# Optimization experiments

Measured on AMD Instinct MI355X. Metric: run time of the kernel, lower is better.

## Reference

```python
import jax, jax.numpy as jnp
import numpy as np

N, E, F, H, C, ED = 10000, 160000, 4, 32, 4, 2  # nodes, edges, in_feat, hidden, classes, edge_dim


def _init(key, shape, fan_in):
    return jax.random.normal(key, shape, jnp.float32) / np.float32(np.sqrt(fan_in))


def setup_inputs() -> dict:
    key = jax.random.key(0)
    ks = iter(jax.random.split(key, 40))
    inp = {
        "x": jax.random.normal(next(ks), (N, F), jnp.float32),
        "edge_index": jax.random.randint(next(ks), (2, E), 0, N, dtype=jnp.int32),
        "edge_attr": jax.random.normal(next(ks), (E, ED), jnp.float32),
    }
    for i, din in enumerate([F, H, H]):
        inp[f"w1_{i}"] = _init(next(ks), (ED, H), ED)
        inp[f"b1_{i}"] = jnp.zeros((H,), jnp.float32)
        inp[f"w2_{i}"] = _init(next(ks), (H, din * H), H)
        inp[f"b2_{i}"] = jnp.zeros((din * H,), jnp.float32)
        inp[f"root_{i}"] = _init(next(ks), (din, H), din)
        inp[f"bias_{i}"] = jnp.zeros((H,), jnp.float32)
    inp["fc_w"] = _init(next(ks), (H, C), H)
    inp["fc_b"] = jnp.zeros((C,), jnp.float32)
    return inp


def _nnconv(x, src, dst, edge_attr, w1, b1, w2, b2, root, bias):
    # edge MLP -> per-edge weight matrix [E, din, H]
    h = jax.nn.relu(edge_attr @ w1 + b1)                      # [E, H]
    W = (h @ w2 + b2).reshape(E, x.shape[1], -1)              # [E, din, H]
    msg = jnp.einsum('ei,eio->eo', x[src], W)                 # gather + per-edge matvec
    agg = jax.ops.segment_sum(msg, dst, num_segments=N)       # scatter-add to targets
    return agg + x @ root + bias                              # root weight + bias (NNConv)


def reference(x, edge_index, edge_attr,
              w1_0, b1_0, w2_0, b2_0, root_0, bias_0,
              w1_1, b1_1, w2_1, b2_1, root_1, bias_1,
              w1_2, b1_2, w2_2, b2_2, root_2, bias_2,
              fc_w, fc_b):
    src, dst = edge_index[0], edge_index[1]
    layers = [(w1_0, b1_0, w2_0, b2_0, root_0, bias_0),
              (w1_1, b1_1, w2_1, b2_1, root_1, bias_1),
              (w1_2, b1_2, w2_2, b2_2, root_2, bias_2)]
    for p in layers:
        x = jax.nn.relu(_nnconv(x, src, dst, edge_attr, *p))  # dropout=0 -> no-op
    logits = x @ fc_w + fc_b
    return jax.nn.log_softmax(logits, axis=1)
```

## Files before the change

kernel.cpp:

```cpp
#include <hip/hip_runtime.h>
#include <hip/hip_bf16.h>
#include <math.h>

#define N_NODES 10000
#define N_EDGES 160000

typedef __attribute__((ext_vector_type(8))) short bf16x8;
typedef __attribute__((ext_vector_type(4))) float f32x4;

static __device__ inline unsigned short f2b(float v) {
    __hip_bfloat16 b = __float2bfloat16(v);
    return *reinterpret_cast<unsigned short*>(&b);
}

__global__ __launch_bounds__(256) void k_tw2z(const float* __restrict__ s0,
                                              const float* __restrict__ s1,
                                              const float* __restrict__ s2,
                                              float* __restrict__ t0,
                                              float* __restrict__ t1,
                                              float* __restrict__ t2,
                                              int* __restrict__ cnt2) {
    int tid = blockIdx.x * 256 + threadIdx.x;
    if (tid < 20480) { cnt2[tid] = 0; return; }
    int d = tid - 20480;
    if (d < 4096) {
        int i = d >> 10, j = d & 1023, o = j >> 5, k = j & 31;
        t0[d] = s0[k * 128 + i * 32 + o];
    } else if (d < 4096 + 32768) {
        int q = d - 4096;
        int i = q >> 10, j = q & 1023, o = j >> 5, k = j & 31;
        t1[q] = s1[k * 1024 + i * 32 + o];
    } else if (d < 4096 + 65536) {
        int q = d - 4096 - 32768;
        int i = q >> 10, j = q & 1023, o = j >> 5, k = j & 31;
        t2[q] = s2[k * 1024 + i * 32 + o];
    }
}

__global__ __launch_bounds__(256) void k_hist(const int* __restrict__ ei,
                                              int* __restrict__ cnt_src,
                                              int* __restrict__ cnt_dst) {
    int e = blockIdx.x * 256 + threadIdx.x;
    if (e >= N_EDGES) return;
    atomicAdd(&cnt_src[ei[e]], 1);
    atomicAdd(&cnt_dst[ei[N_EDGES + e]], 1);
}

__global__ __launch_bounds__(256) void k_scan(const int* __restrict__ cnt_src,
                                              const int* __restrict__ cnt_dst,
                                              int* __restrict__ off_src,
                                              int* __restrict__ off_dst,
                                              int* __restrict__ cur_src,
                                              int* __restrict__ cur_dst) {
    const int* cnt = blockIdx.x == 0 ? cnt_src : cnt_dst;
    int* off = blockIdx.x == 0 ? off_src : off_dst;
    int* cur = blockIdx.x == 0 ? cur_src : cur_dst;
    __shared__ int part[256];
    int t = threadIdx.x;
    int base = t * 40;
    int s = 0;
    for (int i = 0; i < 40; ++i) {
        int idx = base + i;
        if (idx < N_NODES) s += cnt[idx];
    }
    part[t] = s;
    __syncthreads();
    for (int d = 1; d < 256; d <<= 1) {
        int v = (t >= d) ? part[t - d] : 0;
        __syncthreads();
        part[t] += v;
        __syncthreads();
    }
    int run = part[t] - s;
    for (int i = 0; i < 40; ++i) {
        int idx = base + i;
        if (idx < N_NODES) {
            off[idx] = run;
            cur[idx] = run;
            run += cnt[idx];
        }
    }
    if (t == 255) off[N_NODES] = run;
}

__global__ __launch_bounds__(256) void k_scatter_h(const int* __restrict__ ei,
                                                   const float* __restrict__ ea,
                                                   int* __restrict__ cur_src,
                                                   int* __restrict__ cur_dst,
                                                   int* __restrict__ perm,
                                                   const float* __restrict__ w1a, const float* __restrict__ b1a,
                                                   const float* __restrict__ w1b, const float* __restrict__ b1b,
                                                   const float* __restrict__ w1c, const float* __restrict__ b1c,
                                                   unsigned short* __restrict__ h0,
                                                   unsigned short* __restrict__ h1,
                                                   unsigned short* __restrict__ h2) {
    int e = blockIdx.x * 256 + threadIdx.x;
    if (e >= N_EDGES) return;
    float a0 = ea[2 * e], a1 = ea[2 * e + 1];
    int src = ei[e], dst = ei[N_EDGES + e];
    int pos = atomicAdd(&cur_src[src], 1);
    perm[pos] = atomicAdd(&cur_dst[dst], 1);
    const float* W1[3] = {w1a, w1b, w1c};
    const float* B1[3] = {b1a, b1b, b1c};
    unsigned short* H[3] = {h0, h1, h2};
#pragma unroll
    for (int l = 0; l < 3; ++l) {
        unsigned int pk[16];
#pragma unroll
        for (int j = 0; j < 16; ++j) {
            float v0 = fmaxf(a0 * W1[l][2 * j]     + a1 * W1[l][32 + 2 * j]     + B1[l][2 * j],     0.f);
            float v1 = fmaxf(a0 * W1[l][2 * j + 1] + a1 * W1[l][32 + 2 * j + 1] + B1[l][2 * j + 1], 0.f);
            pk[j] = (unsigned int)f2b(v0) | ((unsigned int)f2b(v1) << 16);
        }
        uint4* dp = (uint4*)(H[l] + (size_t)pos * 32);
        dp[0] = make_uint4(pk[0], pk[1], pk[2], pk[3]);
        dp[1] = make_uint4(pk[4], pk[5], pk[6], pk[7]);
        dp[2] = make_uint4(pk[8], pk[9], pk[10], pk[11]);
        dp[3] = make_uint4(pk[12], pk[13], pk[14], pk[15]);
    }
}

template <int DIN, bool FIRST>
__global__ __launch_bounds__(256) void k_G(const float* __restrict__ xin,
                                           const float* __restrict__ w2t,
                                           const float* __restrict__ b2,
                                           const float* __restrict__ root,
                                           const float* __restrict__ bias,
                                           unsigned short* __restrict__ Gb,
                                           float* __restrict__ xb2,
                                           float* __restrict__ agg) {
    const int t = threadIdx.x;
    const int n0 = blockIdx.x * 16;

    __shared__ float xs[16 * DIN];
    for (int idx = t; idx < 16 * DIN; idx += 256) {
        int m = idx / DIN, i = idx - m * DIN;
        float v = xin[(size_t)(n0 + m) * DIN + i];
        if (!FIRST) v = v > 0.f ? v : 0.f;
        xs[idx] = v;
    }
    __syncthreads();

    float acc[16][4];
#pragma unroll
    for (int m = 0; m < 16; ++m)
        acc[m][0] = acc[m][1] = acc[m][2] = acc[m][3] = 0.f;

#pragma unroll
    for (int i = 0; i < DIN; ++i) {
        const float4 w = *(const float4*)(w2t + i * 1024 + t * 4);
#pragma unroll
        for (int m = 0; m < 16; ++m) {
            float xv = xs[m * DIN + i];
            acc[m][0] += xv * w.x;
            acc[m][1] += xv * w.y;
            acc[m][2] += xv * w.z;
            acc[m][3] += xv * w.w;
        }
    }
#pragma unroll
    for (int m = 0; m < 16; ++m) {
        unsigned int p0 = (unsigned int)f2b(acc[m][0]) | ((unsigned int)f2b(acc[m][1]) << 16);
        unsigned int p1 = (unsigned int)f2b(acc[m][2]) | ((unsigned int)f2b(acc[m][3]) << 16);
        *(uint2*)(Gb + (size_t)(n0 + m) * 1024 + t * 4) = make_uint2(p0, p1);
    }

    for (int idx = t; idx < 512; idx += 256) {
        int m = idx >> 5, o = idx & 31;
        float ab = 0.f, ar = bias[o];
#pragma unroll
        for (int i = 0; i < DIN; ++i) {
            float xv = xs[m * DIN + i];
            ab += xv * b2[i * 32 + o];
            ar += xv * root[i * 32 + o];
        }
        size_t p = (size_t)(n0 + m) * 32 + o;
        xb2[p] = ab;
        agg[p] = ar;
    }
}

__global__ __launch_bounds__(256) void k_edge(const int* __restrict__ off_src,
                                              const int* __restrict__ perm,
                                              const unsigned short* __restrict__ hb,
                                              const unsigned short* __restrict__ Gb,
                                              const float* __restrict__ xb2,
                                              float* __restrict__ msgf) {
    int t = threadIdx.x;
    int lane = t & 63;
    int n = blockIdx.x * 4 + (t >> 6);
    int col = lane & 15;
    int quad = lane >> 4;

    const bf16x8 b_lo = *(const bf16x8*)(Gb + (size_t)n * 1024 + col * 32 + quad * 8);
    const bf16x8 b_hi = *(const bf16x8*)(Gb + (size_t)n * 1024 + (col + 16) * 32 + quad * 8);
    float xb_lo = xb2[(size_t)n * 32 + col];
    float xb_hi = xb2[(size_t)n * 32 + 16 + col];

    int jb = off_src[n], je = off_src[n + 1];
    for (int e0 = jb; e0 < je; e0 += 16) {
        int eA = e0 + col;
        bf16x8 afrag = {0, 0, 0, 0, 0, 0, 0, 0};
        if (eA < je) afrag = *(const bf16x8*)(hb + (size_t)eA * 32 + quad * 8);
        f32x4 acc_lo = {xb_lo, xb_lo, xb_lo, xb_lo};
        f32x4 acc_hi = {xb_hi, xb_hi, xb_hi, xb_hi};
        acc_lo = __builtin_amdgcn_mfma_f32_16x16x32_bf16(afrag, b_lo, acc_lo, 0, 0, 0);
        acc_hi = __builtin_amdgcn_mfma_f32_16x16x32_bf16(afrag, b_hi, acc_hi, 0, 0, 0);
#pragma unroll
        for (int r = 0; r < 4; ++r) {
            int er = e0 + quad * 4 + r;
            if (er < je) {
                size_t p = (size_t)perm[er] * 32;
                msgf[p + col] = acc_lo[r];
                msgf[p + 16 + col] = acc_hi[r];
            }
        }
    }
}

__global__ __launch_bounds__(256) void k_agg(const int* __restrict__ off_dst,
                                             const float* __restrict__ msgf,
                                             float* __restrict__ agg) {
    int t = threadIdx.x;
    int n = blockIdx.x * 8 + (t >> 5);
    int o = t & 31;
    int jb = off_dst[n], je = off_dst[n + 1];
    float s = 0.f;
    for (int j = jb; j < je; ++j)
        s += msgf[(size_t)j * 32 + o];
    agg[(size_t)n * 32 + o] += s;
}

__global__ __launch_bounds__(64) void k_final(const float* __restrict__ agg,
                                              const float* __restrict__ fcw,
                                              const float* __restrict__ fcb,
                                              float* __restrict__ out) {
    int n = blockIdx.x * 64 + threadIdx.x;
    if (n >= N_NODES) return;
    float l0 = fcb[0], l1 = fcb[1], l2 = fcb[2], l3 = fcb[3];
#pragma unroll
    for (int o = 0; o < 32; ++o) {
        float xv = agg[(size_t)n * 32 + o];
        xv = xv > 0.f ? xv : 0.f;
        l0 += xv * fcw[o * 4 + 0];
        l1 += xv * fcw[o * 4 + 1];
        l2 += xv * fcw[o * 4 + 2];
        l3 += xv * fcw[o * 4 + 3];
    }
    float m = fmaxf(fmaxf(l0, l1), fmaxf(l2, l3));
    float s = expf(l0 - m) + expf(l1 - m) + expf(l2 - m) + expf(l3 - m);
    float lse = m + logf(s);
    out[(size_t)n * 4 + 0] = l0 - lse;
    out[(size_t)n * 4 + 1] = l1 - lse;
    out[(size_t)n * 4 + 2] = l2 - lse;
    out[(size_t)n * 4 + 3] = l3 - lse;
}

extern "C" void kernel_launch(void* const* d_in, const int* in_sizes, int n_in,
                              void* d_out, int out_size, void* d_ws, size_t ws_size,
                              hipStream_t stream) {
    const float* x0 = (const float*)d_in[0];
    const int*   ei = (const int*)d_in[1];
    const float* ea = (const float*)d_in[2];
    const float *W1[3], *B1[3], *W2[3], *B2[3], *RT[3], *BS[3];
    for (int l = 0; l < 3; ++l) {
        W1[l] = (const float*)d_in[3 + 6 * l];
        B1[l] = (const float*)d_in[4 + 6 * l];
        W2[l] = (const float*)d_in[5 + 6 * l];
        B2[l] = (const float*)d_in[6 + 6 * l];
        RT[l] = (const float*)d_in[7 + 6 * l];
        BS[l] = (const float*)d_in[8 + 6 * l];
    }
    const float* fcw = (const float*)d_in[21];
    const float* fcb = (const float*)d_in[22];
    float* out = (float*)d_out;

    int*   cnt_src = (int*)d_ws;
    int*   cnt_dst = cnt_src + 10240;
    int*   cur_src = cnt_dst + 10240;
    int*   cur_dst = cur_src + 10240;
    int*   off_src = cur_dst + 10240;
    int*   off_dst = off_src + 10240;
    int*   perm    = off_dst + 10240;
    float* w2t0    = (float*)(perm + 163840);
    float* w2t1    = w2t0 + 4096;
    float* w2t2    = w2t1 + 32768;
    float* xb2     = w2t2 + 32768;
    float* aggA    = xb2 + 320000;
    float* aggB    = aggA + 320000;
    float* msgf    = aggB + 320000;
    unsigned short* h0 = (unsigned short*)(msgf + 5120000);
    unsigned short* h1 = h0 + 5120000;
    unsigned short* h2 = h1 + 5120000;
    unsigned short* Gb = h2 + 5120000;

    const int gE256 = (N_EDGES + 255) / 256;
    const int gG    = N_NODES / 16;
    const int gEdge = N_NODES / 4;
    const int gAgg  = N_NODES / 8;

    k_tw2z<<<352, 256, 0, stream>>>(W2[0], W2[1], W2[2], w2t0, w2t1, w2t2, cnt_src);
    k_hist<<<gE256, 256, 0, stream>>>(ei, cnt_src, cnt_dst);
    k_scan<<<2, 256, 0, stream>>>(cnt_src, cnt_dst, off_src, off_dst, cur_src, cur_dst);
    k_scatter_h<<<gE256, 256, 0, stream>>>(ei, ea, cur_src, cur_dst, perm,
                                           W1[0], B1[0], W1[1], B1[1], W1[2], B1[2],
                                           h0, h1, h2);

    k_G<4, true><<<gG, 256, 0, stream>>>(x0, w2t0, B2[0], RT[0], BS[0], Gb, xb2, aggA);
    k_edge<<<gEdge, 256, 0, stream>>>(off_src, perm, h0, Gb, xb2, msgf);
    k_agg<<<gAgg, 256, 0, stream>>>(off_dst, msgf, aggA);

    k_G<32, false><<<gG, 256, 0, stream>>>(aggA, w2t1, B2[1], RT[1], BS[1], Gb, xb2, aggB);
    k_edge<<<gEdge, 256, 0, stream>>>(off_src, perm, h1, Gb, xb2, msgf);
    k_agg<<<gAgg, 256, 0, stream>>>(off_dst, msgf, aggB);

    k_G<32, false><<<gG, 256, 0, stream>>>(aggB, w2t2, B2[2], RT[2], BS[2], Gb, xb2, aggA);
    k_edge<<<gEdge, 256, 0, stream>>>(off_src, perm, h2, Gb, xb2, msgf);
    k_agg<<<gAgg, 256, 0, stream>>>(off_dst, msgf, aggA);

    k_final<<<(N_NODES + 63) / 64, 64, 0, stream>>>(aggA, fcw, fcb, out);
}
```

Measured before the change: 285.5 us.

## Fuse per-node G computation into edge kernel and root/head into aggregation

Removes the separate k_G kernel: each wavefront in k_edge now computes its node's bf16 weight fragment and bias term directly in registers from x and the transposed W2, so the Gb/xb2 buffers are never written or read. The root-weight and bias term moves into k_agg, which also applies ReLU on output, and the final FC plus log-softmax is folded into the last k_agg with a shuffle reduction. This cuts four launches and a few MB of intermediate traffic per layer. In exchange, each of the 64 lanes per node redoes DIN rows of strided float4 W2 loads and register-heavy FMAs, and k_agg recomputes the root matvec once per output lane.

```diff
diff --git a/kernel.cpp b/kernel.cpp
--- a/kernel.cpp
+++ b/kernel.cpp
@@ -13,7 +13,7 @@
     return *reinterpret_cast<unsigned short*>(&b);
 }
 
-__global__ __launch_bounds__(256) void k_tw2z(const float* __restrict__ s0,
+__global__ __launch_bounds__(256) void k_pre0(const float* __restrict__ s0,
                                               const float* __restrict__ s1,
                                               const float* __restrict__ s2,
                                               float* __restrict__ t0,
@@ -120,88 +120,57 @@
     }
 }
 
-template <int DIN, bool FIRST>
-__global__ __launch_bounds__(256) void k_G(const float* __restrict__ xin,
-                                           const float* __restrict__ w2t,
-                                           const float* __restrict__ b2,
-                                           const float* __restrict__ root,
-                                           const float* __restrict__ bias,
-                                           unsigned short* __restrict__ Gb,
-                                           float* __restrict__ xb2,
-                                           float* __restrict__ agg) {
-    const int t = threadIdx.x;
-    const int n0 = blockIdx.x * 16;
-
-    __shared__ float xs[16 * DIN];
-    for (int idx = t; idx < 16 * DIN; idx += 256) {
-        int m = idx / DIN, i = idx - m * DIN;
-        float v = xin[(size_t)(n0 + m) * DIN + i];
-        if (!FIRST) v = v > 0.f ? v : 0.f;
-        xs[idx] = v;
-    }
-    __syncthreads();
-
-    float acc[16][4];
-#pragma unroll
-    for (int m = 0; m < 16; ++m)
-        acc[m][0] = acc[m][1] = acc[m][2] = acc[m][3] = 0.f;
-
-#pragma unroll
-    for (int i = 0; i < DIN; ++i) {
-        const float4 w = *(const float4*)(w2t + i * 1024 + t * 4);
-#pragma unroll
-        for (int m = 0; m < 16; ++m) {
-            float xv = xs[m * DIN + i];
-            acc[m][0] += xv * w.x;
-            acc[m][1] += xv * w.y;
-            acc[m][2] += xv * w.z;
-            acc[m][3] += xv * w.w;
-        }
-    }
-#pragma unroll
-    for (int m = 0; m < 16; ++m) {
-        unsigned int p0 = (unsigned int)f2b(acc[m][0]) | ((unsigned int)f2b(acc[m][1]) << 16);
-        unsigned int p1 = (unsigned int)f2b(acc[m][2]) | ((unsigned int)f2b(acc[m][3]) << 16);
-        *(uint2*)(Gb + (size_t)(n0 + m) * 1024 + t * 4) = make_uint2(p0, p1);
-    }
-
-    for (int idx = t; idx < 512; idx += 256) {
-        int m = idx >> 5, o = idx & 31;
-        float ab = 0.f, ar = bias[o];
-#pragma unroll
-        for (int i = 0; i < DIN; ++i) {
-            float xv = xs[m * DIN + i];
-            ab += xv * b2[i * 32 + o];
-            ar += xv * root[i * 32 + o];
-        }
-        size_t p = (size_t)(n0 + m) * 32 + o;
-        xb2[p] = ab;
-        agg[p] = ar;
-    }
-}
-
-__global__ __launch_bounds__(256) void k_edge(const int* __restrict__ off_src,
+template <int DIN>
+__global__ __launch_bounds__(256) void k_edge(const float* __restrict__ xin,
+                                              const float* __restrict__ w2t,
+                                              const float* __restrict__ b2,
+                                              const int* __restrict__ off_src,
                                               const int* __restrict__ perm,
                                               const unsigned short* __restrict__ hb,
-                                              const unsigned short* __restrict__ Gb,
-                                              const float* __restrict__ xb2,
                                               float* __restrict__ msgf) {
-    int t = threadIdx.x;
-    int lane = t & 63;
-    int n = blockIdx.x * 4 + (t >> 6);
-    int col = lane & 15;
-    int quad = lane >> 4;
-
-    const bf16x8 b_lo = *(const bf16x8*)(Gb + (size_t)n * 1024 + col * 32 + quad * 8);
-    const bf16x8 b_hi = *(const bf16x8*)(Gb + (size_t)n * 1024 + (col + 16) * 32 + quad * 8);
-    float xb_lo = xb2[(size_t)n * 32 + col];
-    float xb_hi = xb2[(size_t)n * 32 + 16 + col];
+    const int t = threadIdx.x;
+    const int lane = t & 63;
+    const int col = lane & 15;
+    const int quad = lane >> 4;
+    const int q8 = quad * 8;
+    const int n = blockIdx.x * 4 + (t >> 6);
+
+    float xv[DIN];
+#pragma unroll
+    for (int i = 0; i < DIN; i += 4) {
+        float4 v = *(const float4*)(xin + (size_t)n * DIN + i);
+        xv[i] = v.x; xv[i + 1] = v.y; xv[i + 2] = v.z; xv[i + 3] = v.w;
+    }
+    float alo[8] = {0, 0, 0, 0, 0, 0, 0, 0};
+    float ahi[8] = {0, 0, 0, 0, 0, 0, 0, 0};
+    float xb_lo = 0.f, xb_hi = 0.f;
+#pragma unroll
+    for (int i = 0; i < DIN; ++i) {
+        const float* wrow = w2t + i * 1024;
+        float4 wl0 = *(const float4*)(wrow + col * 32 + q8);
+        float4 wl1 = *(const float4*)(wrow + col * 32 + q8 + 4);
+        float4 wh0 = *(const float4*)(wrow + (col + 16) * 32 + q8);
+        float4 wh1 = *(const float4*)(wrow + (col + 16) * 32 + q8 + 4);
+        float x = xv[i];
+        alo[0] += x * wl0.x; alo[1] += x * wl0.y; alo[2] += x * wl0.z; alo[3] += x * wl0.w;
+        alo[4] += x * wl1.x; alo[5] += x * wl1.y; alo[6] += x * wl1.z; alo[7] += x * wl1.w;
+        ahi[0] += x * wh0.x; ahi[1] += x * wh0.y; ahi[2] += x * wh0.z; ahi[3] += x * wh0.w;
+        ahi[4] += x * wh1.x; ahi[5] += x * wh1.y; ahi[6] += x * wh1.z; ahi[7] += x * wh1.w;
+        xb_lo += x * b2[i * 32 + col];
+        xb_hi += x * b2[i * 32 + 16 + col];
+    }
+    bf16x8 b_lo, b_hi;
+#pragma unroll
+    for (int j = 0; j < 8; ++j) {
+        b_lo[j] = (short)f2b(alo[j]);
+        b_hi[j] = (short)f2b(ahi[j]);
+    }
 
     int jb = off_src[n], je = off_src[n + 1];
     for (int e0 = jb; e0 < je; e0 += 16) {
         int eA = e0 + col;
         bf16x8 afrag = {0, 0, 0, 0, 0, 0, 0, 0};
-        if (eA < je) afrag = *(const bf16x8*)(hb + (size_t)eA * 32 + quad * 8);
+        if (eA < je) afrag = *(const bf16x8*)(hb + (size_t)eA * 32 + q8);
         f32x4 acc_lo = {xb_lo, xb_lo, xb_lo, xb_lo};
         f32x4 acc_hi = {xb_hi, xb_hi, xb_hi, xb_hi};
         acc_lo = __builtin_amdgcn_mfma_f32_16x16x32_bf16(afrag, b_lo, acc_lo, 0, 0, 0);
@@ -218,42 +187,51 @@
     }
 }
 
-__global__ __launch_bounds__(256) void k_agg(const int* __restrict__ off_dst,
+template <int DIN, bool HEAD>
+__global__ __launch_bounds__(256) void k_agg(const float* __restrict__ xin,
+                                             const float* __restrict__ root,
+                                             const float* __restrict__ bias,
+                                             const int* __restrict__ off_dst,
                                              const float* __restrict__ msgf,
-                                             float* __restrict__ agg) {
-    int t = threadIdx.x;
-    int n = blockIdx.x * 8 + (t >> 5);
-    int o = t & 31;
+                                             const float* __restrict__ fcw,
+                                             const float* __restrict__ fcb,
+                                             float* __restrict__ outp) {
+    const int t = threadIdx.x;
+    const int o = t & 31;
+    const int n = blockIdx.x * 8 + (t >> 5);
+    float s = bias[o];
+#pragma unroll
+    for (int i = 0; i < DIN; ++i)
+        s += xin[(size_t)n * DIN + i] * root[i * 32 + o];
     int jb = off_dst[n], je = off_dst[n + 1];
-    float s = 0.f;
     for (int j = jb; j < je; ++j)
         s += msgf[(size_t)j * 32 + o];
-    agg[(size_t)n * 32 + o] += s;
-}
-
-__global__ __launch_bounds__(64) void k_final(const float* __restrict__ agg,
-                                              const float* __restrict__ fcw,
-                                              const float* __restrict__ fcb,
-                                              float* __restrict__ out) {
-    int n = blockIdx.x * 64 + threadIdx.x;
-    if (n >= N_NODES) return;
-    float l0 = fcb[0], l1 = fcb[1], l2 = fcb[2], l3 = fcb[3];
-#pragma unroll
-    for (int o = 0; o < 32; ++o) {
-        float xv = agg[(size_t)n * 32 + o];
-        xv = xv > 0.f ? xv : 0.f;
-        l0 += xv * fcw[o * 4 + 0];
-        l1 += xv * fcw[o * 4 + 1];
-        l2 += xv * fcw[o * 4 + 2];
-        l3 += xv * fcw[o * 4 + 3];
-    }
-    float m = fmaxf(fmaxf(l0, l1), fmaxf(l2, l3));
-    float s = expf(l0 - m) + expf(l1 - m) + expf(l2 - m) + expf(l3 - m);
-    float lse = m + logf(s);
-    out[(size_t)n * 4 + 0] = l0 - lse;
-    out[(size_t)n * 4 + 1] = l1 - lse;
-    out[(size_t)n * 4 + 2] = l2 - lse;
-    out[(size_t)n * 4 + 3] = l3 - lse;
+    float a = fmaxf(s, 0.f);
+    if (!HEAD) {
+        outp[(size_t)n * 32 + o] = a;
+    } else {
+        float4 p;
+        p.x = a * fcw[o * 4 + 0];
+        p.y = a * fcw[o * 4 + 1];
+        p.z = a * fcw[o * 4 + 2];
+        p.w = a * fcw[o * 4 + 3];
+#pragma unroll
+        for (int m = 16; m >= 1; m >>= 1) {
+            p.x += __shfl_xor(p.x, m, 32);
+            p.y += __shfl_xor(p.y, m, 32);
+            p.z += __shfl_xor(p.z, m, 32);
+            p.w += __shfl_xor(p.w, m, 32);
+        }
+        if (o == 0) {
+            float l0 = p.x + fcb[0], l1 = p.y + fcb[1];
+            float l2 = p.z + fcb[2], l3 = p.w + fcb[3];
+            float mx = fmaxf(fmaxf(l0, l1), fmaxf(l2, l3));
+            float sm = expf(l0 - mx) + expf(l1 - mx) + expf(l2 - mx) + expf(l3 - mx);
+            float lse = mx + logf(sm);
+            *(float4*)(outp + (size_t)n * 4) =
+                make_float4(l0 - lse, l1 - lse, l2 - lse, l3 - lse);
+        }
+    }
 }
 
 extern "C" void kernel_launch(void* const* d_in, const int* in_sizes, int n_in,
@@ -285,38 +263,30 @@
     float* w2t0    = (float*)(perm + 163840);
     float* w2t1    = w2t0 + 4096;
     float* w2t2    = w2t1 + 32768;
-    float* xb2     = w2t2 + 32768;
-    float* aggA    = xb2 + 320000;
+    float* aggA    = w2t2 + 32768;
     float* aggB    = aggA + 320000;
     float* msgf    = aggB + 320000;
     unsigned short* h0 = (unsigned short*)(msgf + 5120000);
     unsigned short* h1 = h0 + 5120000;
     unsigned short* h2 = h1 + 5120000;
-    unsigned short* Gb = h2 + 5120000;
 
     const int gE256 = (N_EDGES + 255) / 256;
-    const int gG    = N_NODES / 16;
     const int gEdge = N_NODES / 4;
     const int gAgg  = N_NODES / 8;
 
-    k_tw2z<<<352, 256, 0, stream>>>(W2[0], W2[1], W2[2], w2t0, w2t1, w2t2, cnt_src);
+    k_pre0<<<352, 256, 0, stream>>>(W2[0], W2[1], W2[2], w2t0, w2t1, w2t2, cnt_src);
     k_hist<<<gE256, 256, 0, stream>>>(ei, cnt_src, cnt_dst);
     k_scan<<<2, 256, 0, stream>>>(cnt_src, cnt_dst, off_src, off_dst, cur_src, cur_dst);
     k_scatter_h<<<gE256, 256, 0, stream>>>(ei, ea, cur_src, cur_dst, perm,
                                            W1[0], B1[0], W1[1], B1[1], W1[2], B1[2],
                                            h0, h1, h2);
 
-    k_G<4, true><<<gG, 256, 0, stream>>>(x0, w2t0, B2[0], RT[0], BS[0], Gb, xb2, aggA);
-    k_edge<<<gEdge, 256, 0, stream>>>(off_src, perm, h0, Gb, xb2, msgf);
-    k_agg<<<gAgg, 256, 0, stream>>>(off_dst, msgf, aggA);
-
-    k_G<32, false><<<gG, 256, 0, stream>>>(aggA, w2t1, B2[1], RT[1], BS[1], Gb, xb2, aggB);
-    k_edge<<<gEdge, 256, 0, stream>>>(off_src, perm, h1, Gb, xb2, msgf);
-    k_agg<<<gAgg, 256, 0, stream>>>(off_dst, msgf, aggB);
-
-    k_G<32, false><<<gG, 256, 0, stream>>>(aggB, w2t2, B2[2], RT[2], BS[2], Gb, xb2, aggA);
-    k_edge<<<gEdge, 256, 0, stream>>>(off_src, perm, h2, Gb, xb2, msgf);
-    k_agg<<<gAgg, 256, 0, stream>>>(off_dst, msgf, aggA);
-
-    k_final<<<(N_NODES + 63) / 64, 64, 0, stream>>>(aggA, fcw, fcb, out);
-}
+    k_edge<4><<<gEdge, 256, 0, stream>>>(x0, w2t0, B2[0], off_src, perm, h0, msgf);
+    k_agg<4, false><<<gAgg, 256, 0, stream>>>(x0, RT[0], BS[0], off_dst, msgf, fcw, fcb, aggA);
+
+    k_edge<32><<<gEdge, 256, 0, stream>>>(aggA, w2t1, B2[1], off_src, perm, h1, msgf);
+    k_agg<32, false><<<gAgg, 256, 0, stream>>>(aggA, RT[1], BS[1], off_dst, msgf, fcw, fcb, aggB);
+
+    k_edge<32><<<gEdge, 256, 0, stream>>>(aggB, w2t2, B2[2], off_src, perm, h2, msgf);
+    k_agg<32, true><<<gAgg, 256, 0, stream>>>(aggB, RT[2], BS[2], off_dst, msgf, fcw, fcb, out);
+}
```

New measurement: 546.8 us. +91.6%, slower.
